# Kernel tuning notes

Hardware: AMD Instinct MI355X
Metric: run time of the kernel (lower is better)

Reference implementation:

```python
import jax, jax.numpy as jnp
import numpy as np

RH, RW = 40, 64          # render image height/width
SAM_HW = 64              # SAM ViT-H feature map spatial size
FEAT_DIM = 17            # voxel_feature_dim
GAUSSIAN_SEM_WEIGHT = 1.0


def nearest_resize(x, oh, ow):
    # torch F.interpolate mode='nearest': idx = floor(out_idx * in/out)
    ih, iw = x.shape[-2], x.shape[-1]
    ri = jnp.floor(jnp.arange(oh) * (ih / oh)).astype(jnp.int32)
    ci = jnp.floor(jnp.arange(ow) * (iw / ow)).astype(jnp.int32)
    return x[..., ri, :][..., ci]


def bilinear_resize(x, oh, ow):
    # torch bilinear, align_corners=False (half-pixel centers)
    ih, iw = x.shape[-2], x.shape[-1]
    def axis(isz, osz):
        src = (jnp.arange(osz, dtype=x.dtype) + 0.5) * (isz / osz) - 0.5
        i0 = jnp.clip(jnp.floor(src), 0, isz - 1).astype(jnp.int32)
        i1 = jnp.clip(i0 + 1, 0, isz - 1)
        w = jnp.clip(src - i0.astype(x.dtype), 0.0, 1.0)
        return i0, i1, w
    r0, r1, wr = axis(ih, oh)
    c0, c1, wc = axis(iw, ow)
    xr = x[..., r0, :] * (1 - wr)[:, None] + x[..., r1, :] * wr[:, None]
    return xr[..., c0] * (1 - wc) + xr[..., c1] * wc


def quat_to_rot(q):  # q: [N,4] normalized (w,x,y,z)
    w, x, y, z = q[:, 0], q[:, 1], q[:, 2], q[:, 3]
    R = jnp.stack([
        1 - 2 * (y * y + z * z), 2 * (x * y - w * z), 2 * (x * z + w * y),
        2 * (x * y + w * z), 1 - 2 * (x * x + z * z), 2 * (y * z - w * x),
        2 * (x * z - w * y), 2 * (y * z + w * x), 1 - 2 * (x * x + y * y)], -1)
    return R.reshape(-1, 3, 3)


def sam_proj(x, W1, b1, g1, be1, W2, b2, g2, be2, W3, b3):
    # Linear -> LayerNorm -> LeakyReLU (x2) -> Linear, all on last dim
    def ln(h, g, b):
        mu = h.mean(-1, keepdims=True)
        var = ((h - mu) ** 2).mean(-1, keepdims=True)
        return (h - mu) / jnp.sqrt(var + 1e-5) * g + b
    h = jax.nn.leaky_relu(ln(x @ W1.T + b1, g1, be1), 0.01)
    h = jax.nn.leaky_relu(ln(h @ W2.T + b2, g2, be2), 0.01)
    return h @ W3.T + b3


def render_feature_map(xyz, feats, opac, scal, quat, vm, intr):
    # Differentiable EWA Gaussian-splat feature rasterizer (3DGS-style math).
    N = xyz.shape[0]
    Rw, t = vm[:3, :3], vm[:3, 3]
    cam = xyz @ Rw.T + t                      # [N,3] camera coords
    x, y, z = cam[:, 0], cam[:, 1], cam[:, 2]
    fx, fy, cx, cy = intr[0], intr[1], intr[2], intr[3]
    zc = jnp.maximum(z, 1e-3)
    u = fx * x / zc + cx
    v = fy * y / zc + cy
    # 3D covariance Sigma = R S S^T R^T, transformed to camera then projected
    Rq = quat_to_rot(quat)
    M = Rq * scal[:, None, :]
    cov3 = M @ jnp.swapaxes(M, 1, 2)          # [N,3,3]
    covw = jnp.einsum('ij,njk,lk->nil', Rw, cov3, Rw)
    inv_z = 1.0 / zc
    zero = jnp.zeros_like(z)
    J = jnp.stack([
        jnp.stack([fx * inv_z, zero, -fx * x * inv_z ** 2], -1),
        jnp.stack([zero, fy * inv_z, -fy * y * inv_z ** 2], -1)], 1)  # [N,2,3]
    cov2 = jnp.einsum('nij,njk,nlk->nil', J, covw, J)
    a = cov2[:, 0, 0] + 0.3
    bq = cov2[:, 0, 1]
    cc = cov2[:, 1, 1] + 0.3
    det = a * cc - bq * bq
    A, Bc, Cc = cc / det, -bq / det, a / det   # conic (inverse 2D cov)
    xx, yy = jnp.meshgrid(jnp.arange(RW, dtype=xyz.dtype), jnp.arange(RH, dtype=xyz.dtype))
    px, py = xx.reshape(-1), yy.reshape(-1)    # [P]
    dx = u[:, None] - px[None, :]              # [N,P]
    dy = v[:, None] - py[None, :]
    power = -0.5 * (A[:, None] * dx * dx + Cc[:, None] * dy * dy) - Bc[:, None] * dx * dy
    alpha = jnp.minimum(0.99, opac * jnp.exp(jnp.minimum(power, 0.0)))
    alpha = alpha * (z > 0.2).astype(alpha.dtype)[:, None]
    # depth-sorted alpha compositing
    order = jnp.argsort(z)
    a_s = alpha[order]                         # [N,P]
    f_s = feats[order]                         # [N,C]
    T = jnp.concatenate([jnp.ones((1, a_s.shape[1]), a_s.dtype),
                         jnp.cumprod(1.0 - a_s, axis=0)[:-1]], axis=0)
    out = jnp.einsum('np,nc->cp', a_s * T, f_s)  # white_background=False -> bg 0
    return out.reshape(FEAT_DIM, RH, RW)


def _forward(voxel_feats, opacity, sam_embd, sam_features, sam_masks, viewmat,
             intrins, pc_xyz, scales, rots, W1, b1, g1, be1, W2, b2, g2, be2, W3, b3):
    B, C = viewmat.shape[0], viewmat.shape[1]
    scal = jnp.exp(scales)
    quat = rots / jnp.linalg.norm(rots, axis=-1, keepdims=True)
    proj = lambda x: sam_proj(x, W1, b1, g1, be1, W2, b2, g2, be2, W3, b3)
    loss_batch = 0.0
    for b in range(B):
        vf = voxel_feats[b].reshape(-1, FEAT_DIM)
        op = opacity[b].reshape(-1, 1)
        loss_c = 0.0
        for c in range(C):
            fmap = render_feature_map(pc_xyz, vf, op, scal, quat, viewmat[b, c], intrins[b, c])
            # use_sam: L1 between rendered map and projected SAM embedding
            se = nearest_resize(sam_embd[b, c], RH, RW)          # [256,RH,RW]
            sed = proj(se.transpose(1, 2, 0))                    # [RH,RW,17]
            loss_c = loss_c + jnp.abs(fmap.transpose(1, 2, 0) - sed).mean()
            # SAM mask contrastive loss
            sf = sam_features[b, c]                              # [256,64,64]
            ldf = proj(sf.reshape(256, -1).T).T.reshape(FEAT_DIM, SAM_HW, SAM_HW)
            masks = sam_masks[b, c]                              # [M,200,200]
            lsm = nearest_resize(masks, SAM_HW, SAM_HW)          # [M,64,64]
            proto = jnp.einsum('mhw,chw->mc', lsm, ldf)
            proto = proto / jnp.maximum(lsm.sum((1, 2)), 1e-6)[:, None]
            prob = jax.nn.sigmoid(jnp.einsum('mc,chw->mhw', proto, fmap))
            frm = bilinear_resize(masks, RH, RW)
            frm = jnp.where(frm <= 0.5, 0.0, frm)
            bce = frm * jnp.log(prob + 1e-8) + (1 - frm) * jnp.log(1 - prob + 1e-8)
            loss_c = loss_c - bce.mean()
        loss_batch = loss_batch + loss_c / C
    return loss_batch / B * GAUSSIAN_SEM_WEIGHT


def setup_inputs() -> dict:
    key = jax.random.key(0)
    ks = jax.random.split(key, 10)
    vs = 2.0
    gx1 = np.arange(-40.0, 40.0 + vs - 0.1, vs)
    gx = (gx1[:40] + gx1[1:41]) / 2
    gy = gx.copy()
    gz1 = np.arange(-2.4, 13.6 + vs - 0.1, vs)
    gz = (gz1[:8] + gz1[1:9]) / 2
    X, Y, Z = np.meshgrid(gx, gy, gz, indexing='ij')
    pc_xyz = np.stack([X, Y, Z], -1).reshape(-1, 3).astype(np.float32)
    N = pc_xyz.shape[0]  # 12800
    # regular grid: 3-NN mean squared dist = vs^2 -> scales = log(sqrt(vs^2))
    scales = np.full((N, 3), np.log(vs), np.float32)
    rots = np.zeros((N, 4), np.float32); rots[:, 0] = 1.0
    vm = np.zeros((1, 2, 4, 4), np.float32)
    vm[0, :, 0, 0] = vm[0, :, 1, 1] = vm[0, :, 2, 2] = vm[0, :, 3, 3] = 1.0
    vm[0, 0, :3, 3] = [0.0, 0.0, 60.0]
    vm[0, 1, :3, 3] = [2.0, -1.0, 62.0]
    intr = np.tile(np.array([32.0, 20.0, 32.0, 20.0], np.float32), (1, 2, 1))
    inp = {
        'voxel_feats': jax.random.normal(ks[0], (1, N, 17), jnp.float32) * 0.5,
        'opacity': jax.random.uniform(ks[1], (1, N, 1), jnp.float32) * 0.1,
        'sam_embd': jax.random.normal(ks[2], (1, 2, 256, 64, 64), jnp.float32),
        'sam_features': jax.random.normal(ks[3], (1, 2, 256, 64, 64), jnp.float32),
        'sam_masks': (jax.random.uniform(ks[4], (1, 2, 16, 200, 200)) < 0.3).astype(jnp.float32),
        'viewmat': jnp.asarray(vm), 'intrins': jnp.asarray(intr),
        'pc_xyz': jnp.asarray(pc_xyz), 'scales': jnp.asarray(scales), 'rots': jnp.asarray(rots),
        'W1': jax.random.normal(ks[5], (64, 256), jnp.float32) * 0.05,
        'b1': jnp.zeros((64,), jnp.float32),
        'g1': jnp.ones((64,), jnp.float32), 'be1': jnp.zeros((64,), jnp.float32),
        'W2': jax.random.normal(ks[6], (64, 64), jnp.float32) * 0.1,
        'b2': jnp.zeros((64,), jnp.float32),
        'g2': jnp.ones((64,), jnp.float32), 'be2': jnp.zeros((64,), jnp.float32),
        'W3': jax.random.normal(ks[7], (17, 64), jnp.float32) * 0.1,
        'b3': jnp.zeros((17,), jnp.float32),
    }
    return inp


def reference(voxel_feats, opacity, sam_embd, sam_features, sam_masks, viewmat,
              intrins, pc_xyz, scales, rots, W1, b1, g1, be1, W2, b2, g2, be2, W3, b3):
    return _forward(voxel_feats, opacity, sam_embd, sam_features, sam_masks, viewmat,
                    intrins, pc_xyz, scales, rots, W1, b1, g1, be1, W2, b2, g2, be2, W3, b3)
```

## Files before the change

kernel.cpp:

```cpp
#include <hip/hip_runtime.h>
#include <math.h>

#define NPTS   12800
#define P_PIX  2560
#define NC     128
#define CHUNK  100
#define NRG    10
#define RANK_CHUNK 400
#define RT     4
#define MLP_PITCH 264

typedef short short8 __attribute__((ext_vector_type(8)));
typedef float f32x4 __attribute__((ext_vector_type(4)));
typedef float f32x2 __attribute__((ext_vector_type(2)));
typedef _Float16 h16x2 __attribute__((ext_vector_type(2)));

union F2H { float f; h16x2 h; unsigned short s[2]; };

__device__ __forceinline__ unsigned short f2bf(float f) {
    unsigned int u = __float_as_uint(f);
    u += 0x7fffu + ((u >> 16) & 1u);
    return (unsigned short)(u >> 16);
}

__device__ __forceinline__ float pack2h(float a, float b) {
    union { float f; _Float16 h[2]; } c;
    c.h[0] = (_Float16)a; c.h[1] = (_Float16)b;
    return c.f;
}
__device__ __forceinline__ float2 unpk2h(float w) {
    union { float f; _Float16 h[2]; } c; c.f = w;
    return make_float2((float)c.h[0], (float)c.h[1]);
}

__global__ __launch_bounds__(256) void prep_kernel(
    const float* __restrict__ xyz, const float* __restrict__ scales,
    const float* __restrict__ rots, const float* __restrict__ opacity,
    const float* __restrict__ viewmat, const float* __restrict__ intrins,
    unsigned long long* __restrict__ keys,
    float* __restrict__ pu, float* __restrict__ pv, float* __restrict__ prad,
    float* __restrict__ phA, float* __restrict__ phC, float* __restrict__ pnB,
    float* __restrict__ pop, int* __restrict__ rnk, float* __restrict__ out, int N) {
    int cam = blockIdx.y;
    int i = blockIdx.x * 256 + threadIdx.x;
    if (i >= N) return;
    int idx = cam * N + i;
    rnk[idx] = 0;
    if (idx == 0) out[0] = 0.0f;
    const float* vm = viewmat + cam * 16;
    const float* it = intrins + cam * 4;
    float fx = it[0], fy = it[1], cx = it[2], cy = it[3];
    float R00 = vm[0], R01 = vm[1], R02 = vm[2], t0 = vm[3];
    float R10 = vm[4], R11 = vm[5], R12 = vm[6], t1 = vm[7];
    float R20 = vm[8], R21 = vm[9], R22 = vm[10], t2 = vm[11];
    float X = xyz[i * 3], Y = xyz[i * 3 + 1], Z = xyz[i * 3 + 2];
    float x = R00 * X + R01 * Y + R02 * Z + t0;
    float y = R10 * X + R11 * Y + R12 * Z + t1;
    float z = R20 * X + R21 * Y + R22 * Z + t2;
    float zc = fmaxf(z, 0.001f);
    float iz = 1.0f / zc;
    float u = fx * x * iz + cx;
    float v = fy * y * iz + cy;
    float qw = rots[i * 4], qx = rots[i * 4 + 1], qy = rots[i * 4 + 2], qz = rots[i * 4 + 3];
    float qn = 1.0f / sqrtf(qw * qw + qx * qx + qy * qy + qz * qz);
    qw *= qn; qx *= qn; qy *= qn; qz *= qn;
    float s0 = expf(scales[i * 3]), s1 = expf(scales[i * 3 + 1]), s2 = expf(scales[i * 3 + 2]);
    float Rq[3][3] = {
        {1 - 2 * (qy * qy + qz * qz), 2 * (qx * qy - qw * qz), 2 * (qx * qz + qw * qy)},
        {2 * (qx * qy + qw * qz), 1 - 2 * (qx * qx + qz * qz), 2 * (qy * qz - qw * qx)},
        {2 * (qx * qz - qw * qy), 2 * (qy * qz + qw * qx), 1 - 2 * (qx * qx + qy * qy)}};
    float M[3][3];
    #pragma unroll
    for (int r = 0; r < 3; ++r) { M[r][0] = Rq[r][0] * s0; M[r][1] = Rq[r][1] * s1; M[r][2] = Rq[r][2] * s2; }
    float c3[3][3];
    #pragma unroll
    for (int a = 0; a < 3; ++a)
        #pragma unroll
        for (int b = 0; b < 3; ++b)
            c3[a][b] = M[a][0] * M[b][0] + M[a][1] * M[b][1] + M[a][2] * M[b][2];
    float Rw[3][3] = {{R00, R01, R02}, {R10, R11, R12}, {R20, R21, R22}};
    float Wt[3][3];
    #pragma unroll
    for (int a = 0; a < 3; ++a)
        #pragma unroll
        for (int b = 0; b < 3; ++b)
            Wt[a][b] = Rw[a][0] * c3[0][b] + Rw[a][1] * c3[1][b] + Rw[a][2] * c3[2][b];
    float cw[3][3];
    #pragma unroll
    for (int a = 0; a < 3; ++a)
        #pragma unroll
        for (int b = 0; b < 3; ++b)
            cw[a][b] = Wt[a][0] * Rw[b][0] + Wt[a][1] * Rw[b][1] + Wt[a][2] * Rw[b][2];
    float j00 = fx * iz, j02 = -fx * x * iz * iz;
    float j11 = fy * iz, j12 = -fy * y * iz * iz;
    float c00 = j00 * j00 * cw[0][0] + 2.0f * j00 * j02 * cw[0][2] + j02 * j02 * cw[2][2];
    float c01 = j00 * j11 * cw[0][1] + j00 * j12 * cw[0][2] + j02 * j11 * cw[2][1] + j02 * j12 * cw[2][2];
    float c11 = j11 * j11 * cw[1][1] + 2.0f * j11 * j12 * cw[1][2] + j12 * j12 * cw[2][2];
    float a = c00 + 0.3f, bq = c01, cc = c11 + 0.3f;
    float det = a * cc - bq * bq;
    float A = cc / det, Bc = -bq / det, Cc = a / det;
    float lmin = 0.5f * ((A + Cc) - sqrtf((A - Cc) * (A - Cc) + 4.0f * Bc * Bc));
    lmin = fmaxf(lmin, 1e-20f);
    float opv = (z > 0.2f) ? opacity[i] : 0.0f;
    float rad = -1.0f;
    if (opv > 0.0f) {
        float tcut = logf(opv) + 18.42f;
        if (tcut > 0.0f) rad = sqrtf(2.0f * tcut / lmin);
    }
    pu[idx] = u; pv[idx] = v; prad[idx] = rad;
    phA[idx] = -0.5f * A; phC[idx] = -0.5f * Cc; pnB[idx] = -Bc;
    pop[idx] = opv;
    unsigned int zb = __float_as_uint(z);
    zb = (zb & 0x80000000u) ? ~zb : (zb | 0x80000000u);
    keys[idx] = ((unsigned long long)zb << 32) | (unsigned int)i;
}

__global__ __launch_bounds__(256) void rank_kernel(const unsigned long long* __restrict__ keys,
                                                   int* __restrict__ rnk, int N) {
    __shared__ unsigned long long sk[RANK_CHUNK];
    int cam = blockIdx.z;
    const unsigned long long* K = keys + (size_t)cam * N;
    int jbase = blockIdx.y * RANK_CHUNK;
    int jcnt = min(RANK_CHUNK, N - jbase);
    for (int t = threadIdx.x; t < jcnt; t += 256) sk[t] = K[jbase + t];
    __syncthreads();
    int i0 = blockIdx.x * (256 * RT) + threadIdx.x;
    unsigned long long ki[RT];
    int cnt[RT];
    #pragma unroll
    for (int t = 0; t < RT; ++t) {
        int i = i0 + t * 256;
        ki[t] = (i < N) ? K[i] : 0xFFFFFFFFFFFFFFFFull;
        cnt[t] = 0;
    }
    #pragma unroll 4
    for (int j = 0; j < jcnt; ++j) {
        unsigned long long kj = sk[j];
        #pragma unroll
        for (int t = 0; t < RT; ++t) cnt[t] += (kj < ki[t]) ? 1 : 0;
    }
    #pragma unroll
    for (int t = 0; t < RT; ++t) {
        int i = i0 + t * 256;
        if (i < N && cnt[t]) atomicAdd(rnk + (size_t)cam * N + i, cnt[t]);
    }
}

__global__ __launch_bounds__(256, 2) void scatter_mlp_kernel(
    const int* __restrict__ rnk,
    const float* __restrict__ pu, const float* __restrict__ pv, const float* __restrict__ prad,
    const float* __restrict__ phA, const float* __restrict__ phC, const float* __restrict__ pnB,
    const float* __restrict__ pop, const float* __restrict__ feats,
    float* __restrict__ rec, float2* __restrict__ vr,
    const float* __restrict__ embd, const float* __restrict__ sfeat,
    const float* __restrict__ W1, const float* __restrict__ b1,
    const float* __restrict__ g1, const float* __restrict__ be1,
    const float* __restrict__ W2, const float* __restrict__ b2,
    const float* __restrict__ g2, const float* __restrict__ be2,
    const float* __restrict__ W3, const float* __restrict__ b3,
    float* __restrict__ sed, float* __restrict__ ldf, int N) {
    __shared__ __align__(16) unsigned short smem[2 * 64 * MLP_PITCH];
    int bid = blockIdx.x;
    int tid = threadIdx.x;
    if (bid < 100) {
        int cam = bid / 50;
        int i = (bid % 50) * 256 + tid;
        if (i >= N) return;
        int idx = cam * N + i;
        int r = rnk[idx];
        float* d = rec + ((size_t)cam * N + r) * 16;
        d[0] = pu[idx]; d[1] = pv[idx];
        d[2] = pack2h(phA[idx], phC[idx]);
        d[3] = pack2h(pnB[idx], pop[idx]);
        const float* f = feats + (size_t)i * 17;
        #pragma unroll
        for (int j = 0; j < 8; ++j) d[4 + j] = pack2h(f[2 * j], f[2 * j + 1]);
        d[12] = pack2h(f[16], 0.0f);
        d[13] = 0.0f; d[14] = 0.0f; d[15] = 0.0f;
        vr[(size_t)cam * N + r] = make_float2(pv[idx], prad[idx]);
        return;
    }
    unsigned short* sX = smem;
    unsigned short* sW = smem + 64 * MLP_PITCH;
    int lane = tid & 63, wv = tid >> 6;
    int m = lane & 15, kq = lane >> 4, q4 = kq * 4;
    int tile = bid - 100;
    const float* xbase;
    if (tile < 80) {
        int cam = tile / 40; int r = tile - cam * 40;
        int ri = (r * 8) / 5;
        xbase = embd + (size_t)cam * 256 * 4096 + ri * 64;
    } else {
        int tt = tile - 80; int cam = tt >> 6;
        xbase = sfeat + (size_t)cam * 256 * 4096 + (tt & 63) * 64;
    }
    const float4* xf4 = (const float4*)xbase;
    for (int idx = tid; idx < 4096; idx += 256) {
        int k = idx >> 4, q = idx & 15;
        float4 xv = xf4[(size_t)k * 1024 + q];
        int r = q * 4;
        sX[(r + 0) * MLP_PITCH + k] = f2bf(xv.x);
        sX[(r + 1) * MLP_PITCH + k] = f2bf(xv.y);
        sX[(r + 2) * MLP_PITCH + k] = f2bf(xv.z);
        sX[(r + 3) * MLP_PITCH + k] = f2bf(xv.w);
    }
    const float4* wf4 = (const float4*)W1;
    for (int idx = tid; idx < 4096; idx += 256) {
        float4 wvv = wf4[idx];
        int n = idx >> 6, kk = (idx & 63) * 4;
        uint2 pk;
        pk.x = (unsigned int)f2bf(wvv.x) | ((unsigned int)f2bf(wvv.y) << 16);
        pk.y = (unsigned int)f2bf(wvv.z) | ((unsigned int)f2bf(wvv.w) << 16);
        *(uint2*)&sW[n * MLP_PITCH + kk] = pk;
    }
    float b1v[4], g1v[4], be1v[4], b2v[4], g2v[4], be2v[4];
    #pragma unroll
    for (int nt = 0; nt < 4; ++nt) {
        int c = nt * 16 + m;
        b1v[nt] = b1[c]; g1v[nt] = g1[c]; be1v[nt] = be1[c];
        b2v[nt] = b2[c]; g2v[nt] = g2[c]; be2v[nt] = be2[c];
    }
    __syncthreads();
    f32x4 acc[4];
    #pragma unroll
    for (int nt = 0; nt < 4; ++nt) acc[nt] = (f32x4){0.f, 0.f, 0.f, 0.f};
    const unsigned short* aptr = sX + (wv * 16 + m) * MLP_PITCH + kq * 8;
    const unsigned short* bptr = sW + m * MLP_PITCH + kq * 8;
    #pragma unroll
    for (int ks = 0; ks < 8; ++ks) {
        short8 af = *(const short8*)(aptr + ks * 32);
        #pragma unroll
        for (int nt = 0; nt < 4; ++nt) {
            short8 bf = *(const short8*)(bptr + nt * 16 * MLP_PITCH + ks * 32);
            acc[nt] = __builtin_amdgcn_mfma_f32_16x16x32_bf16(af, bf, acc[nt], 0, 0, 0);
        }
    }
    __syncthreads();
    unsigned short* hbuf  = smem + wv * 16 * 72;
    unsigned short* hbuf2 = smem + (4 + wv) * 16 * 72;
    unsigned short* W2b = sW;
    unsigned short* W3b = sW + 64 * 72;
    for (int i = tid; i < 4096; i += 256)
        W2b[(i >> 6) * 72 + (i & 63)] = f2bf(W2[i]);
    for (int i = tid; i < 2048; i += 256) {
        int n = i >> 6, k = i & 63;
        W3b[n * 72 + k] = (n < 17) ? f2bf(W3[n * 64 + k]) : 0;
    }
    #pragma unroll
    for (int rg = 0; rg < 4; ++rg) {
        float h0 = acc[0][rg] + b1v[0], h1 = acc[1][rg] + b1v[1];
        float h2 = acc[2][rg] + b1v[2], h3 = acc[3][rg] + b1v[3];
        float s = (h0 + h1) + (h2 + h3);
        s += __shfl_xor(s, 1); s += __shfl_xor(s, 2);
        s += __shfl_xor(s, 4); s += __shfl_xor(s, 8);
        float mu = s * (1.0f / 64.0f);
        float d0 = h0 - mu, d1 = h1 - mu, d2 = h2 - mu, d3 = h3 - mu;
        float vs = (d0 * d0 + d1 * d1) + (d2 * d2 + d3 * d3);
        vs += __shfl_xor(vs, 1); vs += __shfl_xor(vs, 2);
        vs += __shfl_xor(vs, 4); vs += __shfl_xor(vs, 8);
        float rstd = 1.0f / sqrtf(vs * (1.0f / 64.0f) + 1e-5f);
        float hn0 = d0 * rstd * g1v[0] + be1v[0]; hn0 = fmaxf(hn0, 0.01f * hn0);
        float hn1 = d1 * rstd * g1v[1] + be1v[1]; hn1 = fmaxf(hn1, 0.01f * hn1);
        float hn2 = d2 * rstd * g1v[2] + be1v[2]; hn2 = fmaxf(hn2, 0.01f * hn2);
        float hn3 = d3 * rstd * g1v[3] + be1v[3]; hn3 = fmaxf(hn3, 0.01f * hn3);
        int rr = (q4 + rg) * 72 + m;
        hbuf[rr] = f2bf(hn0); hbuf[rr + 16] = f2bf(hn1);
        hbuf[rr + 32] = f2bf(hn2); hbuf[rr + 48] = f2bf(hn3);
    }
    __syncthreads();
    f32x4 acc2[4];
    #pragma unroll
    for (int nt = 0; nt < 4; ++nt) acc2[nt] = (f32x4){0.f, 0.f, 0.f, 0.f};
    const unsigned short* a2p = hbuf + m * 72 + kq * 8;
    #pragma unroll
    for (int ks = 0; ks < 2; ++ks) {
        short8 af = *(const short8*)(a2p + ks * 32);
        #pragma unroll
        for (int nt = 0; nt < 4; ++nt) {
            short8 bf = *(const short8*)(W2b + (nt * 16 + m) * 72 + kq * 8 + ks * 32);
            acc2[nt] = __builtin_amdgcn_mfma_f32_16x16x32_bf16(af, bf, acc2[nt], 0, 0, 0);
        }
    }
    #pragma unroll
    for (int rg = 0; rg < 4; ++rg) {
        float h0 = acc2[0][rg] + b2v[0], h1 = acc2[1][rg] + b2v[1];
        float h2 = acc2[2][rg] + b2v[2], h3 = acc2[3][rg] + b2v[3];
        float s = (h0 + h1) + (h2 + h3);
        s += __shfl_xor(s, 1); s += __shfl_xor(s, 2);
        s += __shfl_xor(s, 4); s += __shfl_xor(s, 8);
        float mu = s * (1.0f / 64.0f);
        float d0 = h0 - mu, d1 = h1 - mu, d2 = h2 - mu, d3 = h3 - mu;
        float vs = (d0 * d0 + d1 * d1) + (d2 * d2 + d3 * d3);
        vs += __shfl_xor(vs, 1); vs += __shfl_xor(vs, 2);
        vs += __shfl_xor(vs, 4); vs += __shfl_xor(vs, 8);
        float rstd = 1.0f / sqrtf(vs * (1.0f / 64.0f) + 1e-5f);
        float hn0 = d0 * rstd * g2v[0] + be2v[0]; hn0 = fmaxf(hn0, 0.01f * hn0);
        float hn1 = d1 * rstd * g2v[1] + be2v[1]; hn1 = fmaxf(hn1, 0.01f * hn1);
        float hn2 = d2 * rstd * g2v[2] + be2v[2]; hn2 = fmaxf(hn2, 0.01f * hn2);
        float hn3 = d3 * rstd * g2v[3] + be2v[3]; hn3 = fmaxf(hn3, 0.01f * hn3);
        int rr = (q4 + rg) * 72 + m;
        hbuf2[rr] = f2bf(hn0); hbuf2[rr + 16] = f2bf(hn1);
        hbuf2[rr + 32] = f2bf(hn2); hbuf2[rr + 48] = f2bf(hn3);
    }
    f32x4 acc3[2];
    acc3[0] = (f32x4){0.f, 0.f, 0.f, 0.f};
    acc3[1] = (f32x4){0.f, 0.f, 0.f, 0.f};
    const unsigned short* a3p = hbuf2 + m * 72 + kq * 8;
    #pragma unroll
    for (int ks = 0; ks < 2; ++ks) {
        short8 af = *(const short8*)(a3p + ks * 32);
        #pragma unroll
        for (int nt = 0; nt < 2; ++nt) {
            short8 bf = *(const short8*)(W3b + (nt * 16 + m) * 72 + kq * 8 + ks * 32);
            acc3[nt] = __builtin_amdgcn_mfma_f32_16x16x32_bf16(af, bf, acc3[nt], 0, 0, 0);
        }
    }
    #pragma unroll
    for (int nt = 0; nt < 2; ++nt) {
        int c = nt * 16 + m;
        if (c < 17) {
            float b3v = b3[c];
            #pragma unroll
            for (int rg = 0; rg < 4; ++rg) {
                int row = tile * 64 + wv * 16 + q4 + rg;
                float val = acc3[nt][rg] + b3v;
                if (row < 5120) {
                    int cam = row / 2560; int p = row - cam * 2560;
                    sed[((size_t)cam * 2560 + p) * 17 + c] = val;
                } else {
                    int rr = row - 5120; int cam = rr >> 12; int t = rr & 4095;
                    ldf[((size_t)cam * 17 + c) * 4096 + t] = val;
                }
            }
        }
    }
}

__global__ __launch_bounds__(64) void splat_kernel(const float* __restrict__ rec,
                                                   const float2* __restrict__ vr,
                                                   float* __restrict__ partT,
                                                   unsigned short* __restrict__ partS, int N) {
    __shared__ __align__(16) float4 sRaw[CHUNK * 4];
    __shared__ __align__(16) float4 sCmp[CHUNK * 4];
    __shared__ unsigned char sIdx[CHUNK];
    int rg = blockIdx.x, ch = blockIdx.y, cam = blockIdx.z;
    int lane = threadIdx.x;
    const float4* src = (const float4*)(rec + ((size_t)cam * N + ch * CHUNK) * 16);
    for (int t = lane; t < CHUNK * 4; t += 64) sRaw[t] = src[t];
    const float2* V = vr + (size_t)cam * N + ch * CHUNK;
    float cy = (float)(rg * 4) + 1.5f;
    int cnt = 0;
    for (int g = 0; g < CHUNK; g += 64) {
        int n = g + lane;
        bool pass = false;
        if (n < CHUNK) {
            float2 t = V[n];
            pass = fabsf(t.x - cy) <= t.y + 1.51f;
        }
        unsigned long long mask = __ballot(pass);
        int pre = __popcll(mask & ((1ull << lane) - 1ull));
        if (pass) sIdx[cnt + pre] = (unsigned char)n;
        cnt += __popcll(mask);
    }
    __syncthreads();
    for (int l = lane; l < cnt; l += 64) {
        int n = sIdx[l];
        sCmp[l * 4 + 0] = sRaw[n * 4 + 0];
        sCmp[l * 4 + 1] = sRaw[n * 4 + 1];
        sCmp[l * 4 + 2] = sRaw[n * 4 + 2];
        sCmp[l * 4 + 3] = sRaw[n * 4 + 3];
    }
    __syncthreads();
    int r0 = rg * 4;
    float px = (float)lane, py0 = (float)r0;
    float T0 = 1.0f, T1 = 1.0f, T2 = 1.0f, T3 = 1.0f;
    h16x2 acc[4][9];
    #pragma unroll
    for (int r = 0; r < 4; ++r)
        #pragma unroll
        for (int j = 0; j < 9; ++j) acc[r][j] = (h16x2){(_Float16)0.f, (_Float16)0.f};
    const float* sRf = (const float*)sCmp;
    for (int i = 0; i < cnt; ++i) {
        const float4* rp = sCmp + i * 4;
        float4 q0 = rp[0];
        float2 g0 = unpk2h(q0.z);
        float2 g1 = unpk2h(q0.w);
        float dx = q0.x - px;
        float dy = q0.y - py0;
        float ta = (g0.x * dx) * dx;
        float tb = g1.x * dx;
        float h2 = g0.y + g0.y;
        float p0 = fmaf(dy, fmaf(g0.y, dy, tb), ta);
        float e = fmaf(-h2, dy, g0.y - tb);
        float p1 = p0 + e; e += h2;
        float p2 = p1 + e; e += h2;
        float p3 = p2 + e;
        float a0 = fminf(0.99f, g1.y * __expf(fminf(p0, 0.0f)));
        float a1 = fminf(0.99f, g1.y * __expf(fminf(p1, 0.0f)));
        float a2 = fminf(0.99f, g1.y * __expf(fminf(p2, 0.0f)));
        float a3 = fminf(0.99f, g1.y * __expf(fminf(p3, 0.0f)));
        float w0 = a0 * T0, w1 = a1 * T1, w2 = a2 * T2, w3 = a3 * T3;
        T0 = fmaf(-T0, a0, T0); T1 = fmaf(-T1, a1, T1);
        T2 = fmaf(-T2, a2, T2); T3 = fmaf(-T3, a3, T3);
        h16x2 wh[4];
        wh[0] = (h16x2){(_Float16)w0, (_Float16)w0};
        wh[1] = (h16x2){(_Float16)w1, (_Float16)w1};
        wh[2] = (h16x2){(_Float16)w2, (_Float16)w2};
        wh[3] = (h16x2){(_Float16)w3, (_Float16)w3};
        float4 q1 = rp[1], q2 = rp[2];
        float fg = sRf[i * 16 + 12];
        F2H f[9];
        f[0].f = q1.x; f[1].f = q1.y; f[2].f = q1.z; f[3].f = q1.w;
        f[4].f = q2.x; f[5].f = q2.y; f[6].f = q2.z; f[7].f = q2.w;
        f[8].f = fg;
        #pragma unroll
        for (int r = 0; r < 4; ++r)
            #pragma unroll
            for (int j = 0; j < 9; ++j)
                acc[r][j] += wh[r] * f[j].h;
    }
    size_t cbase = (size_t)(cam * NC + ch);
    size_t p0i = (size_t)r0 * 64 + lane;
    partT[cbase * P_PIX + p0i]       = T0;
    partT[cbase * P_PIX + p0i + 64]  = T1;
    partT[cbase * P_PIX + p0i + 128] = T2;
    partT[cbase * P_PIX + p0i + 192] = T3;
    #pragma unroll
    for (int r = 0; r < 4; ++r) {
        #pragma unroll
        for (int c = 0; c < 17; ++c) {
            F2H v; v.h = acc[r][c >> 1];
            partS[(cbase * 17 + c) * P_PIX + p0i + (size_t)r * 64] = v.s[c & 1];
        }
    }
}

__global__ __launch_bounds__(256) void combine_proto_kernel(const float* __restrict__ partT,
                                                            const unsigned short* __restrict__ partS,
                                                            const float* __restrict__ masks,
                                                            const float* __restrict__ ldf,
                                                            float* __restrict__ fmap,
                                                            float* __restrict__ proto) {
    __shared__ float red[4][18];
    int bid = blockIdx.x;
    if (bid < 340) {
        int idx = bid * 256 + threadIdx.x;
        int p = idx % P_PIX;
        int rem = idx / P_PIX;
        int c = rem % 17;
        int cam = rem / 17;
        const _Float16* pS = (const _Float16*)partS;
        float acc = 0.0f, Tp = 1.0f;
        #pragma unroll 8
        for (int k = 0; k < NC; ++k) {
            size_t cb = (size_t)(cam * NC + k);
            float Tk = partT[cb * P_PIX + p];
            float S = (float)pS[(cb * 17 + c) * P_PIX + p];
            acc = fmaf(Tp, S, acc);
            Tp *= Tk;
        }
        fmap[((size_t)cam * 17 + c) * P_PIX + p] = acc;
        return;
    }
    int t0 = bid - 340;
    int m = t0 & 15, cam = t0 >> 4;
    const float* M = masks + ((size_t)cam * 16 + m) * 40000;
    float acc[18];
    #pragma unroll
    for (int j = 0; j < 18; ++j) acc[j] = 0.0f;
    for (int t = threadIdx.x; t < 4096; t += 256) {
        int h = t >> 6, w = t & 63;
        int rh = (h * 25) >> 3, rw = (w * 25) >> 3;
        float lv = M[rh * 200 + rw];
        if (lv != 0.0f) {
            acc[17] += lv;
            const float* L = ldf + (size_t)cam * 17 * 4096 + t;
            #pragma unroll
            for (int c = 0; c < 17; ++c) acc[c] = fmaf(lv, L[(size_t)c * 4096], acc[c]);
        }
    }
    int lane = threadIdx.x & 63, wv = threadIdx.x >> 6;
    #pragma unroll
    for (int j = 0; j < 18; ++j) {
        float v = acc[j];
        #pragma unroll
        for (int o = 32; o; o >>= 1) v += __shfl_xor(v, o);
        if (lane == 0) red[wv][j] = v;
    }
    __syncthreads();
    if (threadIdx.x < 17) {
        float sacc = red[0][threadIdx.x] + red[1][threadIdx.x] + red[2][threadIdx.x] + red[3][threadIdx.x];
        float ms = red[0][17] + red[1][17] + red[2][17] + red[3][17];
        proto[((size_t)cam * 16 + m) * 17 + threadIdx.x] = sacc / fmaxf(ms, 1e-6f);
    }
}

__device__ __forceinline__ void block_atomic_add(float v, float* target) {
    #pragma unroll
    for (int o = 32; o; o >>= 1) v += __shfl_xor(v, o);
    __shared__ float sred[4];
    int lane = threadIdx.x & 63, wv = threadIdx.x >> 6;
    if (lane == 0) sred[wv] = v;
    __syncthreads();
    if (threadIdx.x == 0) atomicAdd(target, sred[0] + sred[1] + sred[2] + sred[3]);
}

__global__ __launch_bounds__(256) void bce_kernel(const float* __restrict__ masks,
                                                  const float* __restrict__ proto,
                                                  const float* __restrict__ fmap,
                                                  const float* __restrict__ sed,
                                                  float* __restrict__ out) {
    int idx = blockIdx.x * 256 + threadIdx.x;
    int p = idx % P_PIX;
    int rem = idx / P_PIX;
    int m = rem & 15, cam = rem >> 4;
    const float* pr = proto + ((size_t)cam * 16 + m) * 17;
    float f[17];
    #pragma unroll
    for (int c = 0; c < 17; ++c) f[c] = fmap[((size_t)cam * 17 + c) * P_PIX + p];
    float sdot = 0;
    #pragma unroll
    for (int c = 0; c < 17; ++c) sdot = fmaf(pr[c], f[c], sdot);
    float prob = 1.0f / (1.0f + __expf(-sdot));
    int px = p & 63, py = p >> 6;
    float src_r = (py + 0.5f) * 5.0f - 0.5f;
    float src_c = (px + 0.5f) * 3.125f - 0.5f;
    int r0 = (int)fminf(fmaxf(floorf(src_r), 0.0f), 199.0f);
    int r1 = min(r0 + 1, 199);
    float wr = fminf(fmaxf(src_r - (float)r0, 0.0f), 1.0f);
    int c0 = (int)fminf(fmaxf(floorf(src_c), 0.0f), 199.0f);
    int c1 = min(c0 + 1, 199);
    float wc = fminf(fmaxf(src_c - (float)c0, 0.0f), 1.0f);
    const float* M = masks + ((size_t)cam * 16 + m) * 40000;
    float v00 = M[r0 * 200 + c0], v01 = M[r0 * 200 + c1];
    float v10 = M[r1 * 200 + c0], v11 = M[r1 * 200 + c1];
    float xr0 = v00 * (1.0f - wr) + v10 * wr;
    float xr1 = v01 * (1.0f - wr) + v11 * wr;
    float frm = xr0 * (1.0f - wc) + xr1 * wc;
    frm = (frm <= 0.5f) ? 0.0f : frm;
    float bce = frm * __logf(prob + 1e-8f) + (1.0f - frm) * __logf(1.0f - prob + 1e-8f);
    float val = bce * (-1.0f / (16.0f * 2560.0f * 2.0f));
    if (m == 0) {
        float ssum = 0.0f;
        const float* sp = sed + ((size_t)cam * P_PIX + p) * 17;
        #pragma unroll
        for (int c = 0; c < 17; ++c) ssum += fabsf(f[c] - sp[c]);
        val += ssum * (1.0f / (43520.0f * 2.0f));
    }
    block_atomic_add(val, out);
}

extern "C" void kernel_launch(void* const* d_in, const int* in_sizes, int n_in,
                              void* d_out, int out_size, void* d_ws, size_t ws_size,
                              hipStream_t stream) {
    const float* voxel_feats = (const float*)d_in[0];
    const float* opacity     = (const float*)d_in[1];
    const float* sam_embd    = (const float*)d_in[2];
    const float* sam_features= (const float*)d_in[3];
    const float* sam_masks   = (const float*)d_in[4];
    const float* viewmat     = (const float*)d_in[5];
    const float* intrins     = (const float*)d_in[6];
    const float* pc_xyz      = (const float*)d_in[7];
    const float* scales      = (const float*)d_in[8];
    const float* rots        = (const float*)d_in[9];
    const float* W1 = (const float*)d_in[10], *b1 = (const float*)d_in[11];
    const float* g1 = (const float*)d_in[12], *be1 = (const float*)d_in[13];
    const float* W2 = (const float*)d_in[14], *b2 = (const float*)d_in[15];
    const float* g2 = (const float*)d_in[16], *be2 = (const float*)d_in[17];
    const float* W3 = (const float*)d_in[18], *b3 = (const float*)d_in[19];
    float* out = (float*)d_out;
    const int N = in_sizes[7] / 3;

    char* w = (char*)d_ws;
    size_t off = 0;
    auto alloc = [&](size_t bytes) -> void* {
        off = (off + 255) & ~(size_t)255;
        void* p = w + off; off += bytes; return p;
    };
    int* rnk  = (int*)alloc((size_t)2 * N * sizeof(int));
    unsigned long long* keys = (unsigned long long*)alloc((size_t)2 * N * 8);
    float* params = (float*)alloc((size_t)7 * 2 * N * 4);
    float* pu  = params,           *pv  = params + 2 * N,  *prad = params + 4 * N;
    float* phA = params + 6 * N,   *phC = params + 8 * N,  *pnB  = params + 10 * N;
    float* pop = params + 12 * N;
    float* rec   = (float*)alloc((size_t)2 * N * 16 * 4);
    float2* vr   = (float2*)alloc((size_t)2 * N * 8);
    float* partT = (float*)alloc((size_t)2 * NC * P_PIX * 4);
    unsigned short* partS = (unsigned short*)alloc((size_t)2 * NC * 17 * P_PIX * 2);
    float* fmap  = (float*)alloc((size_t)2 * 17 * P_PIX * 4);
    float* sed   = (float*)alloc((size_t)2 * P_PIX * 17 * 4);
    float* ldf   = (float*)alloc((size_t)2 * 17 * 4096 * 4);
    float* proto = (float*)alloc((size_t)2 * 16 * 17 * 4);

    dim3 gprep((N + 255) / 256, 2);
    prep_kernel<<<gprep, 256, 0, stream>>>(pc_xyz, scales, rots, opacity, viewmat, intrins,
                                           keys, pu, pv, prad, phA, phC, pnB, pop, rnk, out, N);
    dim3 grank((N + 256 * RT - 1) / (256 * RT), (N + RANK_CHUNK - 1) / RANK_CHUNK, 2);
    rank_kernel<<<grank, 256, 0, stream>>>(keys, rnk, N);
    scatter_mlp_kernel<<<308, 256, 0, stream>>>(rnk, pu, pv, prad, phA, phC, pnB, pop,
                                                voxel_feats, rec, vr,
                                                sam_embd, sam_features, W1, b1, g1, be1,
                                                W2, b2, g2, be2, W3, b3, sed, ldf, N);
    dim3 gsplat(NRG, NC, 2);
    splat_kernel<<<gsplat, 64, 0, stream>>>(rec, vr, partT, partS, N);
    combine_proto_kernel<<<372, 256, 0, stream>>>(partT, partS, sam_masks, ldf, fmap, proto);
    bce_kernel<<<(2 * 16 * P_PIX) / 256, 256, 0, stream>>>(sam_masks, proto, fmap, sed, out);
}
```

Baseline: 211.6 us.

## Pack splat partials as half2, move proto into splat grid, truncate bf16 conversions

The splat kernel now writes its per-chunk feature partials as packed half2 words (9 per pixel instead of 17 shorts). The combine kernel reads those pairs, halving its thread count and its number of loads. The mask-prototype reduction moves out of the combine kernel into an extra row of the splat grid, so it runs alongside the splatting, using one 64-lane wave per mask. The MLP's fp32-to-bf16 conversions switch from round-to-nearest to truncation using byte-permute packing, with paired 32-bit LDS stores. Truncation slightly changes numerics, and the proto work now gets far fewer threads per mask.

```diff
diff --git a/kernel.cpp b/kernel.cpp
--- a/kernel.cpp
+++ b/kernel.cpp
@@ -12,17 +12,16 @@
 
 typedef short short8 __attribute__((ext_vector_type(8)));
 typedef float f32x4 __attribute__((ext_vector_type(4)));
-typedef float f32x2 __attribute__((ext_vector_type(2)));
 typedef _Float16 h16x2 __attribute__((ext_vector_type(2)));
 
-union F2H { float f; h16x2 h; unsigned short s[2]; };
-
-__device__ __forceinline__ unsigned short f2bf(float f) {
-    unsigned int u = __float_as_uint(f);
-    u += 0x7fffu + ((u >> 16) & 1u);
-    return (unsigned short)(u >> 16);
-}
-
+union F2H { float f; unsigned int u; h16x2 h; unsigned short s[2]; };
+
+__device__ __forceinline__ unsigned int packbf_tr(float a, float b) {
+    return __builtin_amdgcn_perm(__float_as_uint(b), __float_as_uint(a), 0x07060302u);
+}
+__device__ __forceinline__ unsigned short bf_tr(float a) {
+    return (unsigned short)(__float_as_uint(a) >> 16);
+}
 __device__ __forceinline__ float pack2h(float a, float b) {
     union { float f; _Float16 h[2]; } c;
     c.h[0] = (_Float16)a; c.h[1] = (_Float16)b;
@@ -182,6 +181,8 @@
     }
     unsigned short* sX = smem;
     unsigned short* sW = smem + 64 * MLP_PITCH;
+    unsigned int* sX32 = (unsigned int*)sX;
+    unsigned int* sW32 = (unsigned int*)sW;
     int lane = tid & 63, wv = tid >> 6;
     int m = lane & 15, kq = lane >> 4, q4 = kq * 4;
     int tile = bid - 100;
@@ -195,23 +196,21 @@
         xbase = sfeat + (size_t)cam * 256 * 4096 + (tt & 63) * 64;
     }
     const float4* xf4 = (const float4*)xbase;
-    for (int idx = tid; idx < 4096; idx += 256) {
-        int k = idx >> 4, q = idx & 15;
-        float4 xv = xf4[(size_t)k * 1024 + q];
+    for (int idx = tid; idx < 2048; idx += 256) {
+        int kp = idx >> 4, q = idx & 15;
+        float4 xv0 = xf4[(size_t)(2 * kp) * 1024 + q];
+        float4 xv1 = xf4[(size_t)(2 * kp + 1) * 1024 + q];
         int r = q * 4;
-        sX[(r + 0) * MLP_PITCH + k] = f2bf(xv.x);
-        sX[(r + 1) * MLP_PITCH + k] = f2bf(xv.y);
-        sX[(r + 2) * MLP_PITCH + k] = f2bf(xv.z);
-        sX[(r + 3) * MLP_PITCH + k] = f2bf(xv.w);
-    }
-    const float4* wf4 = (const float4*)W1;
-    for (int idx = tid; idx < 4096; idx += 256) {
-        float4 wvv = wf4[idx];
-        int n = idx >> 6, kk = (idx & 63) * 4;
-        uint2 pk;
-        pk.x = (unsigned int)f2bf(wvv.x) | ((unsigned int)f2bf(wvv.y) << 16);
-        pk.y = (unsigned int)f2bf(wvv.z) | ((unsigned int)f2bf(wvv.w) << 16);
-        *(uint2*)&sW[n * MLP_PITCH + kk] = pk;
+        sX32[(r + 0) * 132 + kp] = packbf_tr(xv0.x, xv1.x);
+        sX32[(r + 1) * 132 + kp] = packbf_tr(xv0.y, xv1.y);
+        sX32[(r + 2) * 132 + kp] = packbf_tr(xv0.z, xv1.z);
+        sX32[(r + 3) * 132 + kp] = packbf_tr(xv0.w, xv1.w);
+    }
+    const float2* wf2 = (const float2*)W1;
+    for (int idx = tid; idx < 8192; idx += 256) {
+        int n = idx >> 7, k2 = idx & 127;
+        float2 wp = wf2[n * 128 + k2];
+        sW32[n * 132 + k2] = packbf_tr(wp.x, wp.y);
     }
     float b1v[4], g1v[4], be1v[4], b2v[4], g2v[4], be2v[4];
     #pragma unroll
@@ -240,11 +239,20 @@
     unsigned short* hbuf2 = smem + (4 + wv) * 16 * 72;
     unsigned short* W2b = sW;
     unsigned short* W3b = sW + 64 * 72;
-    for (int i = tid; i < 4096; i += 256)
-        W2b[(i >> 6) * 72 + (i & 63)] = f2bf(W2[i]);
+    unsigned int* W2b32 = (unsigned int*)W2b;
+    unsigned int* W3b32 = (unsigned int*)W3b;
+    const float2* w2f2 = (const float2*)W2;
     for (int i = tid; i < 2048; i += 256) {
-        int n = i >> 6, k = i & 63;
-        W3b[n * 72 + k] = (n < 17) ? f2bf(W3[n * 64 + k]) : 0;
+        int n = i >> 5, k2 = i & 31;
+        float2 wp = w2f2[n * 32 + k2];
+        W2b32[n * 36 + k2] = packbf_tr(wp.x, wp.y);
+    }
+    const float2* w3f2 = (const float2*)W3;
+    for (int i = tid; i < 1024; i += 256) {
+        int n = i >> 5, k2 = i & 31;
+        unsigned int v = 0;
+        if (n < 17) { float2 wp = w3f2[n * 32 + k2]; v = packbf_tr(wp.x, wp.y); }
+        W3b32[n * 36 + k2] = v;
     }
     #pragma unroll
     for (int rg = 0; rg < 4; ++rg) {
@@ -264,8 +272,8 @@
         float hn2 = d2 * rstd * g1v[2] + be1v[2]; hn2 = fmaxf(hn2, 0.01f * hn2);
         float hn3 = d3 * rstd * g1v[3] + be1v[3]; hn3 = fmaxf(hn3, 0.01f * hn3);
         int rr = (q4 + rg) * 72 + m;
-        hbuf[rr] = f2bf(hn0); hbuf[rr + 16] = f2bf(hn1);
-        hbuf[rr + 32] = f2bf(hn2); hbuf[rr + 48] = f2bf(hn3);
+        hbuf[rr] = bf_tr(hn0); hbuf[rr + 16] = bf_tr(hn1);
+        hbuf[rr + 32] = bf_tr(hn2); hbuf[rr + 48] = bf_tr(hn3);
     }
     __syncthreads();
     f32x4 acc2[4];
@@ -299,8 +307,8 @@
         float hn2 = d2 * rstd * g2v[2] + be2v[2]; hn2 = fmaxf(hn2, 0.01f * hn2);
         float hn3 = d3 * rstd * g2v[3] + be2v[3]; hn3 = fmaxf(hn3, 0.01f * hn3);
         int rr = (q4 + rg) * 72 + m;
-        hbuf2[rr] = f2bf(hn0); hbuf2[rr + 16] = f2bf(hn1);
-        hbuf2[rr + 32] = f2bf(hn2); hbuf2[rr + 48] = f2bf(hn3);
+        hbuf2[rr] = bf_tr(hn0); hbuf2[rr + 16] = bf_tr(hn1);
+        hbuf2[rr + 32] = bf_tr(hn2); hbuf2[rr + 48] = bf_tr(hn3);
     }
     f32x4 acc3[2];
     acc3[0] = (f32x4){0.f, 0.f, 0.f, 0.f};
@@ -339,12 +347,44 @@
 __global__ __launch_bounds__(64) void splat_kernel(const float* __restrict__ rec,
                                                    const float2* __restrict__ vr,
                                                    float* __restrict__ partT,
-                                                   unsigned short* __restrict__ partS, int N) {
+                                                   unsigned int* __restrict__ partS32,
+                                                   const float* __restrict__ masks,
+                                                   const float* __restrict__ ldf,
+                                                   float* __restrict__ proto, int N) {
     __shared__ __align__(16) float4 sRaw[CHUNK * 4];
     __shared__ __align__(16) float4 sCmp[CHUNK * 4];
     __shared__ unsigned char sIdx[CHUNK];
     int rg = blockIdx.x, ch = blockIdx.y, cam = blockIdx.z;
     int lane = threadIdx.x;
+    if (rg == NRG) {
+        int m = ch;
+        if (m >= 16) return;
+        const float* M = masks + ((size_t)cam * 16 + m) * 40000;
+        float acc[18];
+        #pragma unroll
+        for (int j = 0; j < 18; ++j) acc[j] = 0.0f;
+        for (int t = lane; t < 4096; t += 64) {
+            int h = t >> 6, w = t & 63;
+            int rh = (h * 25) >> 3, rw = (w * 25) >> 3;
+            float lv = M[rh * 200 + rw];
+            if (lv != 0.0f) {
+                acc[17] += lv;
+                const float* L = ldf + (size_t)cam * 17 * 4096 + t;
+                #pragma unroll
+                for (int c = 0; c < 17; ++c) acc[c] = fmaf(lv, L[(size_t)c * 4096], acc[c]);
+            }
+        }
+        #pragma unroll
+        for (int j = 0; j < 18; ++j) {
+            float v = acc[j];
+            #pragma unroll
+            for (int o = 32; o; o >>= 1) v += __shfl_xor(v, o);
+            acc[j] = v;
+        }
+        if (lane < 17)
+            proto[((size_t)cam * 16 + m) * 17 + lane] = acc[lane] / fmaxf(acc[17], 1e-6f);
+        return;
+    }
     const float4* src = (const float4*)(rec + ((size_t)cam * N + ch * CHUNK) * 16);
     for (int t = lane; t < CHUNK * 4; t += 64) sRaw[t] = src[t];
     const float2* V = vr + (size_t)cam * N + ch * CHUNK;
@@ -428,71 +468,34 @@
     #pragma unroll
     for (int r = 0; r < 4; ++r) {
         #pragma unroll
-        for (int c = 0; c < 17; ++c) {
-            F2H v; v.h = acc[r][c >> 1];
-            partS[(cbase * 17 + c) * P_PIX + p0i + (size_t)r * 64] = v.s[c & 1];
-        }
-    }
-}
-
-__global__ __launch_bounds__(256) void combine_proto_kernel(const float* __restrict__ partT,
-                                                            const unsigned short* __restrict__ partS,
-                                                            const float* __restrict__ masks,
-                                                            const float* __restrict__ ldf,
-                                                            float* __restrict__ fmap,
-                                                            float* __restrict__ proto) {
-    __shared__ float red[4][18];
-    int bid = blockIdx.x;
-    if (bid < 340) {
-        int idx = bid * 256 + threadIdx.x;
-        int p = idx % P_PIX;
-        int rem = idx / P_PIX;
-        int c = rem % 17;
-        int cam = rem / 17;
-        const _Float16* pS = (const _Float16*)partS;
-        float acc = 0.0f, Tp = 1.0f;
-        #pragma unroll 8
-        for (int k = 0; k < NC; ++k) {
-            size_t cb = (size_t)(cam * NC + k);
-            float Tk = partT[cb * P_PIX + p];
-            float S = (float)pS[(cb * 17 + c) * P_PIX + p];
-            acc = fmaf(Tp, S, acc);
-            Tp *= Tk;
-        }
-        fmap[((size_t)cam * 17 + c) * P_PIX + p] = acc;
-        return;
-    }
-    int t0 = bid - 340;
-    int m = t0 & 15, cam = t0 >> 4;
-    const float* M = masks + ((size_t)cam * 16 + m) * 40000;
-    float acc[18];
-    #pragma unroll
-    for (int j = 0; j < 18; ++j) acc[j] = 0.0f;
-    for (int t = threadIdx.x; t < 4096; t += 256) {
-        int h = t >> 6, w = t & 63;
-        int rh = (h * 25) >> 3, rw = (w * 25) >> 3;
-        float lv = M[rh * 200 + rw];
-        if (lv != 0.0f) {
-            acc[17] += lv;
-            const float* L = ldf + (size_t)cam * 17 * 4096 + t;
-            #pragma unroll
-            for (int c = 0; c < 17; ++c) acc[c] = fmaf(lv, L[(size_t)c * 4096], acc[c]);
-        }
-    }
-    int lane = threadIdx.x & 63, wv = threadIdx.x >> 6;
-    #pragma unroll
-    for (int j = 0; j < 18; ++j) {
-        float v = acc[j];
-        #pragma unroll
-        for (int o = 32; o; o >>= 1) v += __shfl_xor(v, o);
-        if (lane == 0) red[wv][j] = v;
-    }
-    __syncthreads();
-    if (threadIdx.x < 17) {
-        float sacc = red[0][threadIdx.x] + red[1][threadIdx.x] + red[2][threadIdx.x] + red[3][threadIdx.x];
-        float ms = red[0][17] + red[1][17] + red[2][17] + red[3][17];
-        proto[((size_t)cam * 16 + m) * 17 + threadIdx.x] = sacc / fmaxf(ms, 1e-6f);
-    }
+        for (int cp = 0; cp < 9; ++cp) {
+            F2H v; v.h = acc[r][cp];
+            partS32[(cbase * 9 + cp) * P_PIX + p0i + (size_t)r * 64] = v.u;
+        }
+    }
+}
+
+__global__ __launch_bounds__(256) void combine_kernel(const float* __restrict__ partT,
+                                                      const unsigned int* __restrict__ partS32,
+                                                      float* __restrict__ fmap) {
+    int idx = blockIdx.x * 256 + threadIdx.x;
+    int p = idx % P_PIX;
+    int rem = idx / P_PIX;
+    int cp = rem % 9;
+    int cam = rem / 9;
+    float acc0 = 0.0f, acc1 = 0.0f, Tp = 1.0f;
+    #pragma unroll 8
+    for (int k = 0; k < NC; ++k) {
+        size_t cb = (size_t)(cam * NC + k);
+        float Tk = partT[cb * P_PIX + p];
+        F2H v; v.u = partS32[(cb * 9 + cp) * P_PIX + p];
+        acc0 = fmaf(Tp, (float)v.h[0], acc0);
+        acc1 = fmaf(Tp, (float)v.h[1], acc1);
+        Tp *= Tk;
+    }
+    int c = 2 * cp;
+    fmap[((size_t)cam * 17 + c) * P_PIX + p] = acc0;
+    if (c + 1 < 17) fmap[((size_t)cam * 17 + c + 1) * P_PIX + p] = acc1;
 }
 
 __device__ __forceinline__ void block_atomic_add(float v, float* target) {
@@ -586,7 +589,7 @@
     float* rec   = (float*)alloc((size_t)2 * N * 16 * 4);
     float2* vr   = (float2*)alloc((size_t)2 * N * 8);
     float* partT = (float*)alloc((size_t)2 * NC * P_PIX * 4);
-    unsigned short* partS = (unsigned short*)alloc((size_t)2 * NC * 17 * P_PIX * 2);
+    unsigned int* partS32 = (unsigned int*)alloc((size_t)2 * NC * 9 * P_PIX * 4);
     float* fmap  = (float*)alloc((size_t)2 * 17 * P_PIX * 4);
     float* sed   = (float*)alloc((size_t)2 * P_PIX * 17 * 4);
     float* ldf   = (float*)alloc((size_t)2 * 17 * 4096 * 4);
@@ -601,8 +604,9 @@
                                                 voxel_feats, rec, vr,
                                                 sam_embd, sam_features, W1, b1, g1, be1,
                                                 W2, b2, g2, be2, W3, b3, sed, ldf, N);
-    dim3 gsplat(NRG, NC, 2);
-    splat_kernel<<<gsplat, 64, 0, stream>>>(rec, vr, partT, partS, N);
-    combine_proto_kernel<<<372, 256, 0, stream>>>(partT, partS, sam_masks, ldf, fmap, proto);
+    dim3 gsplat(NRG + 1, NC, 2);
+    splat_kernel<<<gsplat, 64, 0, stream>>>(rec, vr, partT, partS32,
+                                            sam_masks, ldf, proto, N);
+    combine_kernel<<<(2 * 9 * P_PIX) / 256, 256, 0, stream>>>(partT, partS32, fmap);
     bce_kernel<<<(2 * 16 * P_PIX) / 256, 256, 0, stream>>>(sam_masks, proto, fmap, sed, out);
 }
```

Result: slower. 227.9 us (+7.7%).
